# Kernel tuning notes

Measured on AMD Instinct MI355X. Metric: run time of the kernel, lower is better.

Reference implementation:

```python
import jax, jax.numpy as jnp
import numpy as np

GAMMA = 0.5
SCALE_BASE = 512.0
LN_EPS = 1e-5


def _xpos(x, downscale=False):
    # x: (B, S, Dh); RetNet XPOS rotary embedding (Jamie-Stirling impl)
    S, Dh = x.shape[1], x.shape[2]
    half = Dh // 2
    base_scale = (jnp.arange(0, Dh, 2, dtype=jnp.float32) + 0.4 * Dh) / (1.4 * Dh)  # (half,)
    power = jnp.arange(S, dtype=jnp.float32)[:, None] / SCALE_BASE                   # (S,1)
    scale = base_scale[None, :] ** power                                             # (S,half)
    inv_freq = 1.0 / (10000.0 ** (jnp.arange(half, dtype=jnp.float32) / half))       # (half,)
    sinusoid = jnp.arange(S, dtype=jnp.float32)[:, None] * inv_freq[None, :]         # (S,half)
    sin, cos = jnp.sin(sinusoid), jnp.cos(sinusoid)
    if downscale:
        scale = 1.0 / scale
    # duplicate_interleave: (S,half) -> (S,Dh) repeating each column twice
    sin_s = jnp.repeat(sin * scale, 2, axis=-1)
    cos_s = jnp.repeat(cos * scale, 2, axis=-1)
    x1, x2 = x[..., ::2], x[..., 1::2]
    rot = jnp.stack((-x2, x1), axis=-1).reshape(x.shape)  # rotate_every_two
    return x * cos_s + rot * sin_s


def _decay_mask(S):
    n = jnp.arange(S)
    diff = (n[:, None] - n[None, :]).astype(jnp.float32)
    return jnp.where(n[:, None] >= n[None, :], GAMMA ** diff, 0.0)  # (S,S)


def setup_inputs() -> dict:
    key = jax.random.key(0)
    ks = jax.random.split(key, 10)
    D, d = 768, 192
    hw, b, s = 196, 8, 32
    x = jax.random.normal(ks[0], (hw, b * s, D), dtype=jnp.float32)
    scale_in = 1.0 / np.sqrt(D)
    scale_d = 1.0 / np.sqrt(d)
    return {
        "x": x,
        "W1": jax.random.normal(ks[1], (D, d), dtype=jnp.float32) * scale_in,
        "b1": jnp.zeros((d,), dtype=jnp.float32),
        "W2": jax.random.normal(ks[2], (d, D), dtype=jnp.float32) * scale_d,
        "b2": jnp.zeros((D,), dtype=jnp.float32),
        "ln_g": jnp.ones((d,), dtype=jnp.float32),
        "ln_b": jnp.zeros((d,), dtype=jnp.float32),
        "WQ": jax.random.normal(ks[3], (d, d), dtype=jnp.float32) * scale_d,
        "WK": jax.random.normal(ks[4], (d, d), dtype=jnp.float32) * scale_d,
        "WV": jax.random.normal(ks[5], (d, d), dtype=jnp.float32) * scale_d,
        "batch_dim": 8,
        "seq_dim": 32,
        "hw": 196,
    }


def reference(x, W1, b1, W2, b2, ln_g, ln_b, WQ, WK, WV, batch_dim, seq_dim, hw):
    D = x.shape[-1]
    # (hw, b*s, D) -> (b*hw, s, D)
    xr = x.reshape(hw, batch_dim, seq_dim, D).transpose(1, 0, 2, 3)
    xr = xr.reshape(batch_dim * hw, seq_dim, D)
    x_down = xr @ W1 + b1  # (B, s, d)
    # LayerNorm
    mu = jnp.mean(x_down, axis=-1, keepdims=True)
    var = jnp.mean((x_down - mu) ** 2, axis=-1, keepdims=True)
    h = (x_down - mu) / jnp.sqrt(var + LN_EPS) * ln_g + ln_b
    # SimpleRetention (parallel form)
    Q = _xpos(h @ WQ, downscale=False)
    K = _xpos(h @ WK, downscale=True)
    V = h @ WV
    Dmask = _decay_mask(seq_dim)  # (s,s)
    att = jnp.einsum("bnd,bmd->bnm", Q, K) * Dmask[None]
    ret = att @ V  # (B, s, d)
    out = xr + (ret @ W2 + b2)
    # (b*hw, s, D) -> (hw, b*s, D)
    out = out.reshape(batch_dim, hw, seq_dim, D).transpose(1, 0, 2, 3)
    return out.reshape(hw, batch_dim * seq_dim, D)
```

## Files before the change

kernel.cpp:

```cpp
#include <hip/hip_runtime.h>

typedef __bf16 bf16x8 __attribute__((ext_vector_type(8)));
typedef __bf16 bf16x4 __attribute__((ext_vector_type(4)));
typedef float floatx4 __attribute__((ext_vector_type(4)));

__device__ __forceinline__ __bf16 f2bf(float f) {
  union { float f; unsigned u; } x; x.f = f;
  unsigned r = (x.u + 0x7FFFu + ((x.u >> 16) & 1u)) >> 16;
  union { unsigned short u; __bf16 b; } o; o.u = (unsigned short)r; return o.b;
}
__device__ __forceinline__ float bf2f(__bf16 b) {
  union { unsigned short u; __bf16 b; } i; i.b = b;
  union { unsigned u; float f; } y; y.u = ((unsigned)i.u) << 16; return y.f;
}

#define MFMA16(a, b, c) __builtin_amdgcn_mfma_f32_16x16x32_bf16(a, b, c, 0, 0, 0)

__global__ __launch_bounds__(256) void prep_weights(
    const float* __restrict__ W1, const float* __restrict__ WQ,
    const float* __restrict__ WK, const float* __restrict__ WV,
    const float* __restrict__ W2,
    __bf16* __restrict__ w1f, __bf16* __restrict__ wqf,
    __bf16* __restrict__ wkf, __bf16* __restrict__ wvf,
    __bf16* __restrict__ w2f) {
  int i = blockIdx.x * 256 + threadIdx.x;
  if (i < 147456) {
    int e = i & 7, lane = (i >> 3) & 63, rest = i >> 9;
    int kk32 = rest % 24, nt = rest / 24;
    int n = nt * 16 + (lane & 15), k = kk32 * 32 + (lane >> 4) * 8 + e;
    w1f[i] = f2bf(W1[k * 192 + n]); return;
  }
  i -= 147456;
  if (i < 36864) {
    int e = i & 7, lane = (i >> 3) & 63, rest = i >> 9;
    int kk32 = rest % 6, nt = rest / 6;
    int n = nt * 16 + (lane & 15), k = kk32 * 32 + (lane >> 4) * 8 + e;
    wqf[i] = f2bf(WQ[k * 192 + n]); return;
  }
  i -= 36864;
  if (i < 36864) {
    int e = i & 7, lane = (i >> 3) & 63, rest = i >> 9;
    int kk32 = rest % 6, nt = rest / 6;
    int n = nt * 16 + (lane & 15), k = kk32 * 32 + (lane >> 4) * 8 + e;
    wkf[i] = f2bf(WK[k * 192 + n]); return;
  }
  i -= 36864;
  if (i < 36864) {
    int e = i & 7, lane = (i >> 3) & 63, rest = i >> 9;
    int kk32 = rest % 6, nt = rest / 6;
    int n = nt * 16 + (lane & 15), k = kk32 * 32 + (lane >> 4) * 8 + e;
    wvf[i] = f2bf(WV[k * 192 + n]); return;
  }
  i -= 36864;
  if (i < 147456) {
    int e = i & 7, lane = (i >> 3) & 63, rest = i >> 9;
    int kk32 = rest % 6, nt = rest / 6;
    int n = nt * 16 + (lane & 15), k = kk32 * 32 + (lane >> 4) * 8 + e;
    w2f[i] = f2bf(W2[k * 768 + n]); return;
  }
}

__global__ __launch_bounds__(256) void prep_xf(
    const float* __restrict__ x, __bf16* __restrict__ xf) {
  int j = blockIdx.x * 256 + threadIdx.x;
  int lane = j & 63;
  int rest = j >> 6;
  int kk32 = rest % 24;
  int rest2 = rest / 24;
  size_t row = (size_t)rest2 * 16 + (lane & 15);
  int d = kk32 * 32 + ((lane >> 4) & 3) * 8;
  const float* src = x + row * 768 + d;
  float4 f0 = *(const float4*)(src);
  float4 f1 = *(const float4*)(src + 4);
  bf16x8 a;
  a[0] = f2bf(f0.x); a[1] = f2bf(f0.y); a[2] = f2bf(f0.z); a[3] = f2bf(f0.w);
  a[4] = f2bf(f1.x); a[5] = f2bf(f1.y); a[6] = f2bf(f1.z); a[7] = f2bf(f1.w);
  *(bf16x8*)(xf + (size_t)j * 8) = a;
}

__global__ __launch_bounds__(256) void prep_tables(
    float* __restrict__ cq, float* __restrict__ sq,
    float* __restrict__ ck, float* __restrict__ sk) {
  int i = blockIdx.x * 256 + threadIdx.x;
  if (i >= 32 * 96) return;
  int s = i / 96, f = i % 96;
  float base = (2.f * f + 0.4f * 192.f) / (1.4f * 192.f);
  float scale = powf(base, (float)s / 512.f);
  float invf = powf(10000.f, -(float)f / 96.f);
  float ang = (float)s * invf;
  float sn = sinf(ang), cs = cosf(ang);
  int o = s * 192 + 2 * f;
  cq[o] = cs * scale; cq[o + 1] = cs * scale;
  sq[o] = sn * scale; sq[o + 1] = sn * scale;
  ck[o] = cs / scale; ck[o + 1] = cs / scale;
  sk[o] = sn / scale; sk[o + 1] = sn / scale;
}

#define SW(r, c) ((r) * 192 + ((c) ^ (((r) & 7) << 3)))

template <bool USE_XF>
__global__ __launch_bounds__(256) void retnet_main(
    const float* __restrict__ x, const float* __restrict__ b1,
    const float* __restrict__ b2, const float* __restrict__ ln_g,
    const float* __restrict__ ln_b,
    const __bf16* __restrict__ w1f, const __bf16* __restrict__ wqf,
    const __bf16* __restrict__ wkf, const __bf16* __restrict__ wvf,
    const __bf16* __restrict__ w2f,
    const float* __restrict__ cq, const float* __restrict__ sq,
    const float* __restrict__ ck, const float* __restrict__ sk,
    const __bf16* __restrict__ xf, float* __restrict__ out) {
  __shared__ __align__(16) char smem[51200];
  __bf16* Q = (__bf16*)smem;
  __bf16* Kl = (__bf16*)(smem + 12288);
  __bf16* Vt = (__bf16*)(smem + 24576);
  __bf16* att = (__bf16*)(smem + 36864);
  __bf16* h = (__bf16*)(smem + 38912);

  const int tid = threadIdx.x;
  const int wv = tid >> 6;
  const int lane = tid & 63;
  const int l16 = lane & 15;
  const int quad = lane >> 4;
  const int kof = quad * 8;
  const int p = blockIdx.x;
  const float* xblk = x + (size_t)p * 32 * 768;

  {
    floatx4 acc[2][3] = {};
    if (USE_XF) {
      const __bf16* xfp = xf + (size_t)p * 24576;
#pragma unroll 4
      for (int kk32 = 0; kk32 < 24; ++kk32) {
        bf16x8 a0 = *(const bf16x8*)(xfp + kk32 * 512 + lane * 8);
        bf16x8 a1 = *(const bf16x8*)(xfp + 12288 + kk32 * 512 + lane * 8);
#pragma unroll
        for (int t = 0; t < 3; ++t) {
          bf16x8 bb = *(const bf16x8*)(w1f + (size_t)((wv * 3 + t) * 24 + kk32) * 512 + lane * 8);
          acc[0][t] = MFMA16(a0, bb, acc[0][t]);
          acc[1][t] = MFMA16(a1, bb, acc[1][t]);
        }
      }
    } else {
      const float* arow0 = xblk + l16 * 768;
      const float* arow1 = xblk + (16 + l16) * 768;
#pragma unroll 2
      for (int kk = 0; kk < 768; kk += 32) {
        float4 f0 = *(const float4*)(arow0 + kk + kof);
        float4 f1 = *(const float4*)(arow0 + kk + kof + 4);
        float4 g0 = *(const float4*)(arow1 + kk + kof);
        float4 g1 = *(const float4*)(arow1 + kk + kof + 4);
        bf16x8 a0, a1;
        a0[0] = f2bf(f0.x); a0[1] = f2bf(f0.y); a0[2] = f2bf(f0.z); a0[3] = f2bf(f0.w);
        a0[4] = f2bf(f1.x); a0[5] = f2bf(f1.y); a0[6] = f2bf(f1.z); a0[7] = f2bf(f1.w);
        a1[0] = f2bf(g0.x); a1[1] = f2bf(g0.y); a1[2] = f2bf(g0.z); a1[3] = f2bf(g0.w);
        a1[4] = f2bf(g1.x); a1[5] = f2bf(g1.y); a1[6] = f2bf(g1.z); a1[7] = f2bf(g1.w);
        int kk32 = kk >> 5;
#pragma unroll
        for (int t = 0; t < 3; ++t) {
          bf16x8 bb = *(const bf16x8*)(w1f + (size_t)((wv * 3 + t) * 24 + kk32) * 512 + lane * 8);
          acc[0][t] = MFMA16(a0, bb, acc[0][t]);
          acc[1][t] = MFMA16(a1, bb, acc[1][t]);
        }
      }
    }
#pragma unroll
    for (int m = 0; m < 2; ++m)
#pragma unroll
      for (int t = 0; t < 3; ++t) {
        int col = wv * 48 + t * 16 + l16;
        float bias = b1[col];
#pragma unroll
        for (int r = 0; r < 4; ++r) {
          int row = m * 16 + quad * 4 + r;
          h[SW(row, col)] = f2bf(acc[m][t][r] + bias);
        }
      }
  }
  __syncthreads();

  {
    int r = tid >> 3, g = tid & 7;
    float vals[24]; float s = 0.f, s2 = 0.f;
#pragma unroll
    for (int j = 0; j < 24; ++j) {
      int c = g * 24 + j;
      float v = bf2f(h[SW(r, c)]);
      vals[j] = v; s += v; s2 += v * v;
    }
#pragma unroll
    for (int o = 1; o < 8; o <<= 1) { s += __shfl_xor(s, o); s2 += __shfl_xor(s2, o); }
    float mu = s * (1.f / 192.f);
    float var = s2 * (1.f / 192.f) - mu * mu;
    float rstd = rsqrtf(var + 1e-5f);
#pragma unroll
    for (int j = 0; j < 24; ++j) {
      int c = g * 24 + j;
      h[SW(r, c)] = f2bf((vals[j] - mu) * rstd * ln_g[c] + ln_b[c]);
    }
  }
  __syncthreads();

  auto gemm_h = [&](const __bf16* __restrict__ Wf, floatx4 (&acc)[2][3]) {
#pragma unroll
    for (int kk32 = 0; kk32 < 6; ++kk32) {
      bf16x8 a0 = *(const bf16x8*)(h + SW(l16, kk32 * 32 + kof));
      bf16x8 a1 = *(const bf16x8*)(h + SW(16 + l16, kk32 * 32 + kof));
#pragma unroll
      for (int t = 0; t < 3; ++t) {
        bf16x8 bb = *(const bf16x8*)(Wf + (size_t)((wv * 3 + t) * 6 + kk32) * 512 + lane * 8);
        acc[0][t] = MFMA16(a0, bb, acc[0][t]);
        acc[1][t] = MFMA16(a1, bb, acc[1][t]);
      }
    }
  };
  {
    floatx4 acc[2][3] = {};
    gemm_h(wqf, acc);
#pragma unroll
    for (int m = 0; m < 2; ++m)
#pragma unroll
      for (int t = 0; t < 3; ++t) {
        int col = wv * 48 + t * 16 + l16;
#pragma unroll
        for (int r = 0; r < 4; ++r) {
          int row = m * 16 + quad * 4 + r;
          float v = acc[m][t][r];
          float pr = __shfl_xor(v, 1);
          float o = v * cq[row * 192 + col] + ((lane & 1) ? pr : -pr) * sq[row * 192 + col];
          Q[SW(row, col)] = f2bf(o);
        }
      }
  }
  {
    floatx4 acc[2][3] = {};
    gemm_h(wkf, acc);
#pragma unroll
    for (int m = 0; m < 2; ++m)
#pragma unroll
      for (int t = 0; t < 3; ++t) {
        int col = wv * 48 + t * 16 + l16;
#pragma unroll
        for (int r = 0; r < 4; ++r) {
          int row = m * 16 + quad * 4 + r;
          float v = acc[m][t][r];
          float pr = __shfl_xor(v, 1);
          float o = v * ck[row * 192 + col] + ((lane & 1) ? pr : -pr) * sk[row * 192 + col];
          Kl[SW(row, col)] = f2bf(o);
        }
      }
  }
  {
    floatx4 acc[2][3] = {};
    gemm_h(wvf, acc);
#pragma unroll
    for (int m = 0; m < 2; ++m)
#pragma unroll
      for (int t = 0; t < 3; ++t) {
        int col = wv * 48 + t * 16 + l16;
        bf16x4 pk;
#pragma unroll
        for (int r = 0; r < 4; ++r) pk[r] = f2bf(acc[m][t][r]);
        *(bf16x4*)(Vt + col * 32 + m * 16 + quad * 4) = pk;
      }
  }
  __syncthreads();

  {
    int mt = wv >> 1, nt = wv & 1;
    floatx4 acc = {0.f, 0.f, 0.f, 0.f};
#pragma unroll
    for (int kk = 0; kk < 192; kk += 32) {
      bf16x8 a = *(const bf16x8*)(Q + SW(mt * 16 + l16, kk + kof));
      bf16x8 bb = *(const bf16x8*)(Kl + SW(nt * 16 + l16, kk + kof));
      acc = MFMA16(a, bb, acc);
    }
#pragma unroll
    for (int r = 0; r < 4; ++r) {
      int i = mt * 16 + quad * 4 + r;
      int j = nt * 16 + l16;
      float v = (i >= j) ? acc[r] * exp2f((float)(j - i)) : 0.f;
      att[i * 32 + j] = f2bf(v);
    }
  }
  __syncthreads();

  {
    floatx4 acc[2][3] = {};
    bf16x8 a0 = *(const bf16x8*)(att + l16 * 32 + kof);
    bf16x8 a1 = *(const bf16x8*)(att + (16 + l16) * 32 + kof);
#pragma unroll
    for (int t = 0; t < 3; ++t) {
      bf16x8 bb = *(const bf16x8*)(Vt + (wv * 48 + t * 16 + l16) * 32 + kof);
      acc[0][t] = MFMA16(a0, bb, acc[0][t]);
      acc[1][t] = MFMA16(a1, bb, acc[1][t]);
    }
#pragma unroll
    for (int m = 0; m < 2; ++m)
#pragma unroll
      for (int t = 0; t < 3; ++t) {
        int col = wv * 48 + t * 16 + l16;
#pragma unroll
        for (int r = 0; r < 4; ++r) {
          int row = m * 16 + quad * 4 + r;
          h[SW(row, col)] = f2bf(acc[m][t][r]);
        }
      }
  }
  __syncthreads();

  {
    bf16x8 af[2][6];
#pragma unroll
    for (int k6 = 0; k6 < 6; ++k6) {
      af[0][k6] = *(const bf16x8*)(h + SW(l16, k6 * 32 + kof));
      af[1][k6] = *(const bf16x8*)(h + SW(16 + l16, k6 * 32 + kof));
    }
#pragma unroll
    for (int g = 0; g < 4; ++g) {
      floatx4 acc[2][3] = {};
#pragma unroll
      for (int k6 = 0; k6 < 6; ++k6) {
#pragma unroll
        for (int t = 0; t < 3; ++t) {
          bf16x8 bb = *(const bf16x8*)(w2f + (size_t)((wv * 12 + g * 3 + t) * 6 + k6) * 512 + lane * 8);
          acc[0][t] = MFMA16(af[0][k6], bb, acc[0][t]);
          acc[1][t] = MFMA16(af[1][k6], bb, acc[1][t]);
        }
      }
#pragma unroll
      for (int m = 0; m < 2; ++m)
#pragma unroll
        for (int t = 0; t < 3; ++t) {
          int col = wv * 192 + g * 48 + t * 16 + l16;
          float bias = b2[col];
#pragma unroll
          for (int r = 0; r < 4; ++r) {
            int row = m * 16 + quad * 4 + r;
            size_t gi = (size_t)p * 24576 + row * 768 + col;
            out[gi] = xblk[row * 768 + col] + acc[m][t][r] + bias;
          }
        }
    }
  }
}

extern "C" void kernel_launch(void* const* d_in, const int* in_sizes, int n_in,
                              void* d_out, int out_size, void* d_ws, size_t ws_size,
                              hipStream_t stream) {
  const float* x = (const float*)d_in[0];
  const float* W1 = (const float*)d_in[1];
  const float* b1 = (const float*)d_in[2];
  const float* W2 = (const float*)d_in[3];
  const float* b2 = (const float*)d_in[4];
  const float* lng = (const float*)d_in[5];
  const float* lnb = (const float*)d_in[6];
  const float* WQ = (const float*)d_in[7];
  const float* WK = (const float*)d_in[8];
  const float* WV = (const float*)d_in[9];
  float* out = (float*)d_out;

  char* ws = (char*)d_ws;
  __bf16* w1f = (__bf16*)(ws + 0);
  __bf16* wqf = (__bf16*)(ws + 294912);
  __bf16* wkf = (__bf16*)(ws + 368640);
  __bf16* wvf = (__bf16*)(ws + 442368);
  __bf16* w2f = (__bf16*)(ws + 516096);
  float* cq = (float*)(ws + 811008);
  float* sq = cq + 6144;
  float* ck = sq + 6144;
  float* sk = ck + 6144;
  const size_t xf_off = 909312;
  const size_t xf_bytes = 77070336;
  bool use_xf = (ws_size >= xf_off + xf_bytes);
  __bf16* xfp = (__bf16*)(ws + xf_off);

  hipLaunchKernelGGL(prep_weights, dim3(1584), dim3(256), 0, stream,
                     W1, WQ, WK, WV, W2, w1f, wqf, wkf, wvf, w2f);
  hipLaunchKernelGGL(prep_tables, dim3(12), dim3(256), 0, stream, cq, sq, ck, sk);
  if (use_xf) {
    hipLaunchKernelGGL(prep_xf, dim3(18816), dim3(256), 0, stream, x, xfp);
    hipLaunchKernelGGL((retnet_main<true>), dim3(1568), dim3(256), 0, stream,
                       x, b1, b2, lng, lnb, w1f, wqf, wkf, wvf, w2f,
                       cq, sq, ck, sk, (const __bf16*)xfp, out);
  } else {
    hipLaunchKernelGGL((retnet_main<false>), dim3(1568), dim3(256), 0, stream,
                       x, b1, b2, lng, lnb, w1f, wqf, wkf, wvf, w2f,
                       cq, sq, ck, sk, (const __bf16*)nullptr, out);
  }
}
```

Before: 452.0 us.

## Fuse x bf16 conversion into main kernel with double-buffered LDS staging

Drops the separate prep_xf pass, which wrote a bf16 copy of x to workspace and read it back. The main kernel now loads fp32 x in chunks, converts it, and stages it into LDS in MFMA fragment order, double-buffered across the Q/K regions so the next chunk's global loads overlap the current chunk's MFMAs. All LDS tiles switch from swizzled row-major to a fragment-native layout, the attention matrix reuses the Q buffer so LDS shrinks, and launch bounds request 3 blocks per CU. The cost is extra barriers inside the first GEMM and more register pressure from the in-flight loads.

```diff
diff --git a/kernel.cpp b/kernel.cpp
--- a/kernel.cpp
+++ b/kernel.cpp
@@ -12,6 +12,17 @@
 __device__ __forceinline__ float bf2f(__bf16 b) {
   union { unsigned short u; __bf16 b; } i; i.b = b;
   union { unsigned u; float f; } y; y.u = ((unsigned)i.u) << 16; return y.f;
+}
+__device__ __forceinline__ bf16x8 cvt8(float4 f0, float4 f1) {
+  bf16x8 v;
+  v[0] = f2bf(f0.x); v[1] = f2bf(f0.y); v[2] = f2bf(f0.z); v[3] = f2bf(f0.w);
+  v[4] = f2bf(f1.x); v[5] = f2bf(f1.y); v[6] = f2bf(f1.z); v[7] = f2bf(f1.w);
+  return v;
+}
+
+__device__ __forceinline__ int afoff(int row, int col, int Kb) {
+  return ((((row >> 4) * Kb + (col >> 5)) * 64 + ((col >> 3) & 3) * 16 + (row & 15)) << 4)
+         + ((col & 7) << 1);
 }
 
 #define MFMA16(a, b, c) __builtin_amdgcn_mfma_f32_16x16x32_bf16(a, b, c, 0, 0, 0)
@@ -58,24 +69,6 @@
     int n = nt * 16 + (lane & 15), k = kk32 * 32 + (lane >> 4) * 8 + e;
     w2f[i] = f2bf(W2[k * 768 + n]); return;
   }
-}
-
-__global__ __launch_bounds__(256) void prep_xf(
-    const float* __restrict__ x, __bf16* __restrict__ xf) {
-  int j = blockIdx.x * 256 + threadIdx.x;
-  int lane = j & 63;
-  int rest = j >> 6;
-  int kk32 = rest % 24;
-  int rest2 = rest / 24;
-  size_t row = (size_t)rest2 * 16 + (lane & 15);
-  int d = kk32 * 32 + ((lane >> 4) & 3) * 8;
-  const float* src = x + row * 768 + d;
-  float4 f0 = *(const float4*)(src);
-  float4 f1 = *(const float4*)(src + 4);
-  bf16x8 a;
-  a[0] = f2bf(f0.x); a[1] = f2bf(f0.y); a[2] = f2bf(f0.z); a[3] = f2bf(f0.w);
-  a[4] = f2bf(f1.x); a[5] = f2bf(f1.y); a[6] = f2bf(f1.z); a[7] = f2bf(f1.w);
-  *(bf16x8*)(xf + (size_t)j * 8) = a;
 }
 
 __global__ __launch_bounds__(256) void prep_tables(
@@ -96,10 +89,7 @@
   sk[o] = sn / scale; sk[o + 1] = sn / scale;
 }
 
-#define SW(r, c) ((r) * 192 + ((c) ^ (((r) & 7) << 3)))
-
-template <bool USE_XF>
-__global__ __launch_bounds__(256) void retnet_main(
+__global__ __launch_bounds__(256, 3) void retnet_main(
     const float* __restrict__ x, const float* __restrict__ b1,
     const float* __restrict__ b2, const float* __restrict__ ln_g,
     const float* __restrict__ ln_b,
@@ -108,59 +98,72 @@
     const __bf16* __restrict__ w2f,
     const float* __restrict__ cq, const float* __restrict__ sq,
     const float* __restrict__ ck, const float* __restrict__ sk,
-    const __bf16* __restrict__ xf, float* __restrict__ out) {
-  __shared__ __align__(16) char smem[51200];
-  __bf16* Q = (__bf16*)smem;
-  __bf16* Kl = (__bf16*)(smem + 12288);
-  __bf16* Vt = (__bf16*)(smem + 24576);
-  __bf16* att = (__bf16*)(smem + 36864);
-  __bf16* h = (__bf16*)(smem + 38912);
+    float* __restrict__ out) {
+  __shared__ __align__(16) char smem[49152];
+  char* Qb = smem;
+  char* Kb = smem + 12288;
+  char* Vtb = smem + 24576;
+  char* hb = smem + 36864;
 
   const int tid = threadIdx.x;
   const int wv = tid >> 6;
   const int lane = tid & 63;
   const int l16 = lane & 15;
   const int quad = lane >> 4;
-  const int kof = quad * 8;
+  const int lane16 = lane << 4;
+  const int wv3 = wv * 3;
   const int p = blockIdx.x;
-  const float* xblk = x + (size_t)p * 32 * 768;
-
-  {
-    floatx4 acc[2][3] = {};
-    if (USE_XF) {
-      const __bf16* xfp = xf + (size_t)p * 24576;
-#pragma unroll 4
-      for (int kk32 = 0; kk32 < 24; ++kk32) {
-        bf16x8 a0 = *(const bf16x8*)(xfp + kk32 * 512 + lane * 8);
-        bf16x8 a1 = *(const bf16x8*)(xfp + 12288 + kk32 * 512 + lane * 8);
+  const float* xblk = x + (size_t)p * 24576;
+
+  const int srow = tid >> 3;
+  const int scol8 = (tid & 7) * 8;
+  const float* sbase = xblk + srow * 768 + scol8;
+  const int wo0 = ((((srow >> 4) * 6 + (scol8 >> 5)) * 64 +
+                    ((scol8 >> 3) & 3) * 16 + (srow & 15)) << 4);
+  const char* w1b = (const char*)w1f;
+
+  floatx4 acc[2][3] = {};
+  {
+    {
+      float4 L[6];
+#pragma unroll
+      for (int g = 0; g < 3; ++g) {
+        const float* a = sbase + g * 64;
+        L[2 * g] = *(const float4*)a; L[2 * g + 1] = *(const float4*)(a + 4);
+      }
+#pragma unroll
+      for (int g = 0; g < 3; ++g)
+        *(bf16x8*)(Qb + wo0 + g * 2048) = cvt8(L[2 * g], L[2 * g + 1]);
+    }
+    __syncthreads();
+#pragma unroll
+    for (int c = 0; c < 4; ++c) {
+      char* rb = (c & 1) ? Kb : Qb;
+      char* wb = (c & 1) ? Qb : Kb;
+      float4 L[6];
+      if (c < 3) {
+#pragma unroll
+        for (int g = 0; g < 3; ++g) {
+          const float* a = sbase + (c + 1) * 192 + g * 64;
+          L[2 * g] = *(const float4*)a; L[2 * g + 1] = *(const float4*)(a + 4);
+        }
+      }
+#pragma unroll
+      for (int kkc = 0; kkc < 6; ++kkc) {
+        bf16x8 a0 = *(const bf16x8*)(rb + kkc * 1024 + lane16);
+        bf16x8 a1 = *(const bf16x8*)(rb + (6 + kkc) * 1024 + lane16);
 #pragma unroll
         for (int t = 0; t < 3; ++t) {
-          bf16x8 bb = *(const bf16x8*)(w1f + (size_t)((wv * 3 + t) * 24 + kk32) * 512 + lane * 8);
+          bf16x8 bb = *(const bf16x8*)(w1b + (size_t)((wv3 + t) * 24 + c * 6 + kkc) * 1024 + lane16);
           acc[0][t] = MFMA16(a0, bb, acc[0][t]);
           acc[1][t] = MFMA16(a1, bb, acc[1][t]);
         }
       }
-    } else {
-      const float* arow0 = xblk + l16 * 768;
-      const float* arow1 = xblk + (16 + l16) * 768;
-#pragma unroll 2
-      for (int kk = 0; kk < 768; kk += 32) {
-        float4 f0 = *(const float4*)(arow0 + kk + kof);
-        float4 f1 = *(const float4*)(arow0 + kk + kof + 4);
-        float4 g0 = *(const float4*)(arow1 + kk + kof);
-        float4 g1 = *(const float4*)(arow1 + kk + kof + 4);
-        bf16x8 a0, a1;
-        a0[0] = f2bf(f0.x); a0[1] = f2bf(f0.y); a0[2] = f2bf(f0.z); a0[3] = f2bf(f0.w);
-        a0[4] = f2bf(f1.x); a0[5] = f2bf(f1.y); a0[6] = f2bf(f1.z); a0[7] = f2bf(f1.w);
-        a1[0] = f2bf(g0.x); a1[1] = f2bf(g0.y); a1[2] = f2bf(g0.z); a1[3] = f2bf(g0.w);
-        a1[4] = f2bf(g1.x); a1[5] = f2bf(g1.y); a1[6] = f2bf(g1.z); a1[7] = f2bf(g1.w);
-        int kk32 = kk >> 5;
-#pragma unroll
-        for (int t = 0; t < 3; ++t) {
-          bf16x8 bb = *(const bf16x8*)(w1f + (size_t)((wv * 3 + t) * 24 + kk32) * 512 + lane * 8);
-          acc[0][t] = MFMA16(a0, bb, acc[0][t]);
-          acc[1][t] = MFMA16(a1, bb, acc[1][t]);
-        }
+      if (c < 3) {
+#pragma unroll
+        for (int g = 0; g < 3; ++g)
+          *(bf16x8*)(wb + wo0 + g * 2048) = cvt8(L[2 * g], L[2 * g + 1]);
+        __syncthreads();
       }
     }
 #pragma unroll
@@ -172,7 +175,7 @@
 #pragma unroll
         for (int r = 0; r < 4; ++r) {
           int row = m * 16 + quad * 4 + r;
-          h[SW(row, col)] = f2bf(acc[m][t][r] + bias);
+          *(__bf16*)(hb + afoff(row, col, 6)) = f2bf(acc[m][t][r] + bias);
         }
       }
   }
@@ -184,7 +187,7 @@
 #pragma unroll
     for (int j = 0; j < 24; ++j) {
       int c = g * 24 + j;
-      float v = bf2f(h[SW(r, c)]);
+      float v = bf2f(*(const __bf16*)(hb + afoff(r, c, 6)));
       vals[j] = v; s += v; s2 += v * v;
     }
 #pragma unroll
@@ -195,27 +198,28 @@
 #pragma unroll
     for (int j = 0; j < 24; ++j) {
       int c = g * 24 + j;
-      h[SW(r, c)] = f2bf((vals[j] - mu) * rstd * ln_g[c] + ln_b[c]);
-    }
-  }
-  __syncthreads();
-
-  auto gemm_h = [&](const __bf16* __restrict__ Wf, floatx4 (&acc)[2][3]) {
-#pragma unroll
-    for (int kk32 = 0; kk32 < 6; ++kk32) {
-      bf16x8 a0 = *(const bf16x8*)(h + SW(l16, kk32 * 32 + kof));
-      bf16x8 a1 = *(const bf16x8*)(h + SW(16 + l16, kk32 * 32 + kof));
-#pragma unroll
-      for (int t = 0; t < 3; ++t) {
-        bf16x8 bb = *(const bf16x8*)(Wf + (size_t)((wv * 3 + t) * 6 + kk32) * 512 + lane * 8);
-        acc[0][t] = MFMA16(a0, bb, acc[0][t]);
-        acc[1][t] = MFMA16(a1, bb, acc[1][t]);
+      *(__bf16*)(hb + afoff(r, c, 6)) = f2bf((vals[j] - mu) * rstd * ln_g[c] + ln_b[c]);
+    }
+  }
+  __syncthreads();
+
+  auto gemm_h = [&](const __bf16* __restrict__ Wf, floatx4(&a)[2][3]) {
+    const char* wc = (const char*)Wf;
+#pragma unroll
+    for (int kk = 0; kk < 6; ++kk) {
+      bf16x8 a0 = *(const bf16x8*)(hb + kk * 1024 + lane16);
+      bf16x8 a1 = *(const bf16x8*)(hb + (6 + kk) * 1024 + lane16);
+#pragma unroll
+      for (int t = 0; t < 3; ++t) {
+        bf16x8 bb = *(const bf16x8*)(wc + (size_t)((wv3 + t) * 6 + kk) * 1024 + lane16);
+        a[0][t] = MFMA16(a0, bb, a[0][t]);
+        a[1][t] = MFMA16(a1, bb, a[1][t]);
       }
     }
   };
   {
-    floatx4 acc[2][3] = {};
-    gemm_h(wqf, acc);
+    floatx4 aq[2][3] = {};
+    gemm_h(wqf, aq);
 #pragma unroll
     for (int m = 0; m < 2; ++m)
 #pragma unroll
@@ -224,16 +228,16 @@
 #pragma unroll
         for (int r = 0; r < 4; ++r) {
           int row = m * 16 + quad * 4 + r;
-          float v = acc[m][t][r];
+          float v = aq[m][t][r];
           float pr = __shfl_xor(v, 1);
           float o = v * cq[row * 192 + col] + ((lane & 1) ? pr : -pr) * sq[row * 192 + col];
-          Q[SW(row, col)] = f2bf(o);
-        }
-      }
-  }
-  {
-    floatx4 acc[2][3] = {};
-    gemm_h(wkf, acc);
+          *(__bf16*)(Qb + afoff(row, col, 6)) = f2bf(o);
+        }
+      }
+  }
+  {
+    floatx4 ak[2][3] = {};
+    gemm_h(wkf, ak);
 #pragma unroll
     for (int m = 0; m < 2; ++m)
 #pragma unroll
@@ -242,57 +246,59 @@
 #pragma unroll
         for (int r = 0; r < 4; ++r) {
           int row = m * 16 + quad * 4 + r;
-          float v = acc[m][t][r];
+          float v = ak[m][t][r];
           float pr = __shfl_xor(v, 1);
           float o = v * ck[row * 192 + col] + ((lane & 1) ? pr : -pr) * sk[row * 192 + col];
-          Kl[SW(row, col)] = f2bf(o);
-        }
-      }
-  }
-  {
-    floatx4 acc[2][3] = {};
-    gemm_h(wvf, acc);
-#pragma unroll
-    for (int m = 0; m < 2; ++m)
-#pragma unroll
-      for (int t = 0; t < 3; ++t) {
-        int col = wv * 48 + t * 16 + l16;
+          *(__bf16*)(Kb + afoff(row, col, 6)) = f2bf(o);
+        }
+      }
+  }
+  {
+    floatx4 av[2][3] = {};
+    gemm_h(wvf, av);
+#pragma unroll
+    for (int m = 0; m < 2; ++m)
+#pragma unroll
+      for (int t = 0; t < 3; ++t) {
+        int d = wv * 48 + t * 16 + l16;
+        int s0 = m * 16 + quad * 4;
         bf16x4 pk;
 #pragma unroll
-        for (int r = 0; r < 4; ++r) pk[r] = f2bf(acc[m][t][r]);
-        *(bf16x4*)(Vt + col * 32 + m * 16 + quad * 4) = pk;
+        for (int r = 0; r < 4; ++r) pk[r] = f2bf(av[m][t][r]);
+        *(bf16x4*)(Vtb + afoff(d, s0, 1)) = pk;
       }
   }
   __syncthreads();
 
   {
     int mt = wv >> 1, nt = wv & 1;
-    floatx4 acc = {0.f, 0.f, 0.f, 0.f};
-#pragma unroll
-    for (int kk = 0; kk < 192; kk += 32) {
-      bf16x8 a = *(const bf16x8*)(Q + SW(mt * 16 + l16, kk + kof));
-      bf16x8 bb = *(const bf16x8*)(Kl + SW(nt * 16 + l16, kk + kof));
-      acc = MFMA16(a, bb, acc);
-    }
+    floatx4 a4 = {0.f, 0.f, 0.f, 0.f};
+#pragma unroll
+    for (int kk = 0; kk < 6; ++kk) {
+      bf16x8 a = *(const bf16x8*)(Qb + (mt * 6 + kk) * 1024 + lane16);
+      bf16x8 bb = *(const bf16x8*)(Kb + (nt * 6 + kk) * 1024 + lane16);
+      a4 = MFMA16(a, bb, a4);
+    }
+    __syncthreads();
 #pragma unroll
     for (int r = 0; r < 4; ++r) {
       int i = mt * 16 + quad * 4 + r;
       int j = nt * 16 + l16;
-      float v = (i >= j) ? acc[r] * exp2f((float)(j - i)) : 0.f;
-      att[i * 32 + j] = f2bf(v);
-    }
-  }
-  __syncthreads();
-
-  {
-    floatx4 acc[2][3] = {};
-    bf16x8 a0 = *(const bf16x8*)(att + l16 * 32 + kof);
-    bf16x8 a1 = *(const bf16x8*)(att + (16 + l16) * 32 + kof);
+      float v = (i >= j) ? a4[r] * exp2f((float)(j - i)) : 0.f;
+      *(__bf16*)(Qb + afoff(i, j, 1)) = f2bf(v);
+    }
+  }
+  __syncthreads();
+
+  {
+    floatx4 ar[2][3] = {};
+    bf16x8 a0 = *(const bf16x8*)(Qb + lane16);
+    bf16x8 a1 = *(const bf16x8*)(Qb + 1024 + lane16);
 #pragma unroll
     for (int t = 0; t < 3; ++t) {
-      bf16x8 bb = *(const bf16x8*)(Vt + (wv * 48 + t * 16 + l16) * 32 + kof);
-      acc[0][t] = MFMA16(a0, bb, acc[0][t]);
-      acc[1][t] = MFMA16(a1, bb, acc[1][t]);
+      bf16x8 bb = *(const bf16x8*)(Vtb + (wv3 + t) * 1024 + lane16);
+      ar[0][t] = MFMA16(a0, bb, ar[0][t]);
+      ar[1][t] = MFMA16(a1, bb, ar[1][t]);
     }
 #pragma unroll
     for (int m = 0; m < 2; ++m)
@@ -302,29 +308,30 @@
 #pragma unroll
         for (int r = 0; r < 4; ++r) {
           int row = m * 16 + quad * 4 + r;
-          h[SW(row, col)] = f2bf(acc[m][t][r]);
-        }
-      }
-  }
-  __syncthreads();
-
-  {
+          *(__bf16*)(hb + afoff(row, col, 6)) = f2bf(ar[m][t][r]);
+        }
+      }
+  }
+  __syncthreads();
+
+  {
+    const char* w2b = (const char*)w2f;
     bf16x8 af[2][6];
 #pragma unroll
     for (int k6 = 0; k6 < 6; ++k6) {
-      af[0][k6] = *(const bf16x8*)(h + SW(l16, k6 * 32 + kof));
-      af[1][k6] = *(const bf16x8*)(h + SW(16 + l16, k6 * 32 + kof));
+      af[0][k6] = *(const bf16x8*)(hb + k6 * 1024 + lane16);
+      af[1][k6] = *(const bf16x8*)(hb + (6 + k6) * 1024 + lane16);
     }
 #pragma unroll
     for (int g = 0; g < 4; ++g) {
-      floatx4 acc[2][3] = {};
+      floatx4 ao[2][3] = {};
 #pragma unroll
       for (int k6 = 0; k6 < 6; ++k6) {
 #pragma unroll
         for (int t = 0; t < 3; ++t) {
-          bf16x8 bb = *(const bf16x8*)(w2f + (size_t)((wv * 12 + g * 3 + t) * 6 + k6) * 512 + lane * 8);
-          acc[0][t] = MFMA16(af[0][k6], bb, acc[0][t]);
-          acc[1][t] = MFMA16(af[1][k6], bb, acc[1][t]);
+          bf16x8 bb = *(const bf16x8*)(w2b + (size_t)((wv * 12 + g * 3 + t) * 6 + k6) * 1024 + lane16);
+          ao[0][t] = MFMA16(af[0][k6], bb, ao[0][t]);
+          ao[1][t] = MFMA16(af[1][k6], bb, ao[1][t]);
         }
       }
 #pragma unroll
@@ -337,7 +344,7 @@
           for (int r = 0; r < 4; ++r) {
             int row = m * 16 + quad * 4 + r;
             size_t gi = (size_t)p * 24576 + row * 768 + col;
-            out[gi] = xblk[row * 768 + col] + acc[m][t][r] + bias;
+            out[gi] = xblk[row * 768 + col] + ao[m][t][r] + bias;
           }
         }
     }
@@ -369,22 +376,11 @@
   float* sq = cq + 6144;
   float* ck = sq + 6144;
   float* sk = ck + 6144;
-  const size_t xf_off = 909312;
-  const size_t xf_bytes = 77070336;
-  bool use_xf = (ws_size >= xf_off + xf_bytes);
-  __bf16* xfp = (__bf16*)(ws + xf_off);
 
   hipLaunchKernelGGL(prep_weights, dim3(1584), dim3(256), 0, stream,
                      W1, WQ, WK, WV, W2, w1f, wqf, wkf, wvf, w2f);
   hipLaunchKernelGGL(prep_tables, dim3(12), dim3(256), 0, stream, cq, sq, ck, sk);
-  if (use_xf) {
-    hipLaunchKernelGGL(prep_xf, dim3(18816), dim3(256), 0, stream, x, xfp);
-    hipLaunchKernelGGL((retnet_main<true>), dim3(1568), dim3(256), 0, stream,
-                       x, b1, b2, lng, lnb, w1f, wqf, wkf, wvf, w2f,
-                       cq, sq, ck, sk, (const __bf16*)xfp, out);
-  } else {
-    hipLaunchKernelGGL((retnet_main<false>), dim3(1568), dim3(256), 0, stream,
-                       x, b1, b2, lng, lnb, w1f, wqf, wkf, wvf, w2f,
-                       cq, sq, ck, sk, (const __bf16*)nullptr, out);
-  }
-}
+  hipLaunchKernelGGL(retnet_main, dim3(1568), dim3(256), 0, stream,
+                     x, b1, b2, lng, lnb, w1f, wqf, wkf, wvf, w2f,
+                     cq, sq, ck, sk, out);
+}
```

New measurement: 525.3 us. 1.16x slower.

## Process two sequences per block and stage prep_xf through shared memory

Applied to the files above, without the earlier changes.

The main kernel now handles two 32-row sequences per workgroup, so each weight fragment loaded from global memory feeds twice as many MFMAs. LDS buffers are doubled and reused across phases (V and h share storage, ret and Q share storage), and V is held in registers across a barrier. prep_xf now reads each 32x768 tile with coalesced float4 loads into a swizzled LDS tile, then writes it out in fragment order. Trade-offs: larger LDS use (about 78 KB) and more registers can lower occupancy, and the grid halves to 784 blocks.

```diff
diff --git a/kernel.cpp b/kernel.cpp
--- a/kernel.cpp
+++ b/kernel.cpp
@@ -15,6 +15,9 @@
 }
 
 #define MFMA16(a, b, c) __builtin_amdgcn_mfma_f32_16x16x32_bf16(a, b, c, 0, 0, 0)
+
+#define SW(r, c) ((r) * 192 + ((c) ^ (((r) & 7) << 3)))
+#define SWX(r, c) ((r) * 768 + ((c) ^ (((r) & 7) << 3)))
 
 __global__ __launch_bounds__(256) void prep_weights(
     const float* __restrict__ W1, const float* __restrict__ WQ,
@@ -62,20 +65,30 @@
 
 __global__ __launch_bounds__(256) void prep_xf(
     const float* __restrict__ x, __bf16* __restrict__ xf) {
-  int j = blockIdx.x * 256 + threadIdx.x;
-  int lane = j & 63;
-  int rest = j >> 6;
-  int kk32 = rest % 24;
-  int rest2 = rest / 24;
-  size_t row = (size_t)rest2 * 16 + (lane & 15);
-  int d = kk32 * 32 + ((lane >> 4) & 3) * 8;
-  const float* src = x + row * 768 + d;
-  float4 f0 = *(const float4*)(src);
-  float4 f1 = *(const float4*)(src + 4);
-  bf16x8 a;
-  a[0] = f2bf(f0.x); a[1] = f2bf(f0.y); a[2] = f2bf(f0.z); a[3] = f2bf(f0.w);
-  a[4] = f2bf(f1.x); a[5] = f2bf(f1.y); a[6] = f2bf(f1.z); a[7] = f2bf(f1.w);
-  *(bf16x8*)(xf + (size_t)j * 8) = a;
+  __shared__ __align__(16) __bf16 tile[24576];
+  int p = blockIdx.x;
+  int tid = threadIdx.x;
+  const float* xb = x + (size_t)p * 24576;
+#pragma unroll
+  for (int i = 0; i < 24; ++i) {
+    int idx = i * 256 + tid;
+    float4 v = ((const float4*)xb)[idx];
+    int row = idx / 192, c4 = (idx % 192) * 4;
+    bf16x4 b;
+    b[0] = f2bf(v.x); b[1] = f2bf(v.y); b[2] = f2bf(v.z); b[3] = f2bf(v.w);
+    *(bf16x4*)(&tile[SWX(row, c4)]) = b;
+  }
+  __syncthreads();
+  __bf16* dst = xf + (size_t)p * 24576;
+#pragma unroll
+  for (int w = 0; w < 12; ++w) {
+    int j = w * 256 + tid;
+    int lane = j & 63, rest = j >> 6;
+    int kk32 = rest % 24, mt = rest / 24;
+    int row = mt * 16 + (lane & 15);
+    int col = kk32 * 32 + ((lane >> 4) & 3) * 8;
+    *(bf16x8*)(dst + j * 8) = *(const bf16x8*)(&tile[SWX(row, col)]);
+  }
 }
 
 __global__ __launch_bounds__(256) void prep_tables(
@@ -96,10 +109,8 @@
   sk[o] = sn / scale; sk[o + 1] = sn / scale;
 }
 
-#define SW(r, c) ((r) * 192 + ((c) ^ (((r) & 7) << 3)))
-
 template <bool USE_XF>
-__global__ __launch_bounds__(256) void retnet_main(
+__global__ __launch_bounds__(256, 2) void retnet_main(
     const float* __restrict__ x, const float* __restrict__ b1,
     const float* __restrict__ b2, const float* __restrict__ ln_g,
     const float* __restrict__ ln_b,
@@ -109,12 +120,13 @@
     const float* __restrict__ cq, const float* __restrict__ sq,
     const float* __restrict__ ck, const float* __restrict__ sk,
     const __bf16* __restrict__ xf, float* __restrict__ out) {
-  __shared__ __align__(16) char smem[51200];
-  __bf16* Q = (__bf16*)smem;
-  __bf16* Kl = (__bf16*)(smem + 12288);
-  __bf16* Vt = (__bf16*)(smem + 24576);
-  __bf16* att = (__bf16*)(smem + 36864);
-  __bf16* h = (__bf16*)(smem + 38912);
+  __shared__ __align__(16) char smem[79872];
+  __bf16* h[2] = {(__bf16*)smem, (__bf16*)(smem + 12288)};
+  __bf16* Q[2] = {(__bf16*)(smem + 24576), (__bf16*)(smem + 36864)};
+  __bf16* K[2] = {(__bf16*)(smem + 49152), (__bf16*)(smem + 61440)};
+  __bf16* att[2] = {(__bf16*)(smem + 73728), (__bf16*)(smem + 76800)};
+  __bf16** Vt = h;
+  __bf16** ret = Q;
 
   const int tid = threadIdx.x;
   const int wv = tid >> 6;
@@ -122,224 +134,267 @@
   const int l16 = lane & 15;
   const int quad = lane >> 4;
   const int kof = quad * 8;
+  const int wv3 = wv * 3;
   const int p = blockIdx.x;
-  const float* xblk = x + (size_t)p * 32 * 768;
-
-  {
-    floatx4 acc[2][3] = {};
+  const float* xblk[2] = {x + (size_t)(2 * p) * 24576, x + (size_t)(2 * p + 1) * 24576};
+
+  {
+    floatx4 acc[2][2][3] = {};
     if (USE_XF) {
-      const __bf16* xfp = xf + (size_t)p * 24576;
+      const __bf16* xf0 = xf + (size_t)(2 * p) * 24576;
 #pragma unroll 4
       for (int kk32 = 0; kk32 < 24; ++kk32) {
-        bf16x8 a0 = *(const bf16x8*)(xfp + kk32 * 512 + lane * 8);
-        bf16x8 a1 = *(const bf16x8*)(xfp + 12288 + kk32 * 512 + lane * 8);
-#pragma unroll
-        for (int t = 0; t < 3; ++t) {
-          bf16x8 bb = *(const bf16x8*)(w1f + (size_t)((wv * 3 + t) * 24 + kk32) * 512 + lane * 8);
-          acc[0][t] = MFMA16(a0, bb, acc[0][t]);
-          acc[1][t] = MFMA16(a1, bb, acc[1][t]);
+        bf16x8 a[2][2];
+#pragma unroll
+        for (int ss = 0; ss < 2; ++ss) {
+          a[ss][0] = *(const bf16x8*)(xf0 + ss * 24576 + kk32 * 512 + lane * 8);
+          a[ss][1] = *(const bf16x8*)(xf0 + ss * 24576 + 12288 + kk32 * 512 + lane * 8);
+        }
+#pragma unroll
+        for (int t = 0; t < 3; ++t) {
+          bf16x8 bb = *(const bf16x8*)(w1f + (size_t)((wv3 + t) * 24 + kk32) * 512 + lane * 8);
+          acc[0][0][t] = MFMA16(a[0][0], bb, acc[0][0][t]);
+          acc[0][1][t] = MFMA16(a[0][1], bb, acc[0][1][t]);
+          acc[1][0][t] = MFMA16(a[1][0], bb, acc[1][0][t]);
+          acc[1][1][t] = MFMA16(a[1][1], bb, acc[1][1][t]);
         }
       }
     } else {
-      const float* arow0 = xblk + l16 * 768;
-      const float* arow1 = xblk + (16 + l16) * 768;
 #pragma unroll 2
       for (int kk = 0; kk < 768; kk += 32) {
-        float4 f0 = *(const float4*)(arow0 + kk + kof);
-        float4 f1 = *(const float4*)(arow0 + kk + kof + 4);
-        float4 g0 = *(const float4*)(arow1 + kk + kof);
-        float4 g1 = *(const float4*)(arow1 + kk + kof + 4);
-        bf16x8 a0, a1;
-        a0[0] = f2bf(f0.x); a0[1] = f2bf(f0.y); a0[2] = f2bf(f0.z); a0[3] = f2bf(f0.w);
-        a0[4] = f2bf(f1.x); a0[5] = f2bf(f1.y); a0[6] = f2bf(f1.z); a0[7] = f2bf(f1.w);
-        a1[0] = f2bf(g0.x); a1[1] = f2bf(g0.y); a1[2] = f2bf(g0.z); a1[3] = f2bf(g0.w);
-        a1[4] = f2bf(g1.x); a1[5] = f2bf(g1.y); a1[6] = f2bf(g1.z); a1[7] = f2bf(g1.w);
+        bf16x8 a[2][2];
+#pragma unroll
+        for (int ss = 0; ss < 2; ++ss)
+#pragma unroll
+          for (int m = 0; m < 2; ++m) {
+            const float* ar = xblk[ss] + (m * 16 + l16) * 768 + kk + kof;
+            float4 f0 = *(const float4*)ar;
+            float4 f1 = *(const float4*)(ar + 4);
+            bf16x8 v;
+            v[0] = f2bf(f0.x); v[1] = f2bf(f0.y); v[2] = f2bf(f0.z); v[3] = f2bf(f0.w);
+            v[4] = f2bf(f1.x); v[5] = f2bf(f1.y); v[6] = f2bf(f1.z); v[7] = f2bf(f1.w);
+            a[ss][m] = v;
+          }
         int kk32 = kk >> 5;
 #pragma unroll
         for (int t = 0; t < 3; ++t) {
-          bf16x8 bb = *(const bf16x8*)(w1f + (size_t)((wv * 3 + t) * 24 + kk32) * 512 + lane * 8);
-          acc[0][t] = MFMA16(a0, bb, acc[0][t]);
-          acc[1][t] = MFMA16(a1, bb, acc[1][t]);
-        }
-      }
-    }
-#pragma unroll
-    for (int m = 0; m < 2; ++m)
-#pragma unroll
-      for (int t = 0; t < 3; ++t) {
-        int col = wv * 48 + t * 16 + l16;
-        float bias = b1[col];
-#pragma unroll
-        for (int r = 0; r < 4; ++r) {
-          int row = m * 16 + quad * 4 + r;
-          h[SW(row, col)] = f2bf(acc[m][t][r] + bias);
-        }
-      }
-  }
-  __syncthreads();
-
-  {
-    int r = tid >> 3, g = tid & 7;
-    float vals[24]; float s = 0.f, s2 = 0.f;
-#pragma unroll
-    for (int j = 0; j < 24; ++j) {
-      int c = g * 24 + j;
-      float v = bf2f(h[SW(r, c)]);
-      vals[j] = v; s += v; s2 += v * v;
-    }
-#pragma unroll
-    for (int o = 1; o < 8; o <<= 1) { s += __shfl_xor(s, o); s2 += __shfl_xor(s2, o); }
-    float mu = s * (1.f / 192.f);
-    float var = s2 * (1.f / 192.f) - mu * mu;
-    float rstd = rsqrtf(var + 1e-5f);
-#pragma unroll
-    for (int j = 0; j < 24; ++j) {
-      int c = g * 24 + j;
-      h[SW(r, c)] = f2bf((vals[j] - mu) * rstd * ln_g[c] + ln_b[c]);
-    }
-  }
-  __syncthreads();
-
-  auto gemm_h = [&](const __bf16* __restrict__ Wf, floatx4 (&acc)[2][3]) {
-#pragma unroll
-    for (int kk32 = 0; kk32 < 6; ++kk32) {
-      bf16x8 a0 = *(const bf16x8*)(h + SW(l16, kk32 * 32 + kof));
-      bf16x8 a1 = *(const bf16x8*)(h + SW(16 + l16, kk32 * 32 + kof));
-#pragma unroll
-      for (int t = 0; t < 3; ++t) {
-        bf16x8 bb = *(const bf16x8*)(Wf + (size_t)((wv * 3 + t) * 6 + kk32) * 512 + lane * 8);
-        acc[0][t] = MFMA16(a0, bb, acc[0][t]);
-        acc[1][t] = MFMA16(a1, bb, acc[1][t]);
-      }
-    }
-  };
-  {
-    floatx4 acc[2][3] = {};
-    gemm_h(wqf, acc);
-#pragma unroll
-    for (int m = 0; m < 2; ++m)
-#pragma unroll
-      for (int t = 0; t < 3; ++t) {
-        int col = wv * 48 + t * 16 + l16;
-#pragma unroll
-        for (int r = 0; r < 4; ++r) {
-          int row = m * 16 + quad * 4 + r;
-          float v = acc[m][t][r];
-          float pr = __shfl_xor(v, 1);
-          float o = v * cq[row * 192 + col] + ((lane & 1) ? pr : -pr) * sq[row * 192 + col];
-          Q[SW(row, col)] = f2bf(o);
-        }
-      }
-  }
-  {
-    floatx4 acc[2][3] = {};
-    gemm_h(wkf, acc);
-#pragma unroll
-    for (int m = 0; m < 2; ++m)
-#pragma unroll
-      for (int t = 0; t < 3; ++t) {
-        int col = wv * 48 + t * 16 + l16;
-#pragma unroll
-        for (int r = 0; r < 4; ++r) {
-          int row = m * 16 + quad * 4 + r;
-          float v = acc[m][t][r];
-          float pr = __shfl_xor(v, 1);
-          float o = v * ck[row * 192 + col] + ((lane & 1) ? pr : -pr) * sk[row * 192 + col];
-          Kl[SW(row, col)] = f2bf(o);
-        }
-      }
-  }
-  {
-    floatx4 acc[2][3] = {};
-    gemm_h(wvf, acc);
-#pragma unroll
-    for (int m = 0; m < 2; ++m)
-#pragma unroll
-      for (int t = 0; t < 3; ++t) {
-        int col = wv * 48 + t * 16 + l16;
-        bf16x4 pk;
-#pragma unroll
-        for (int r = 0; r < 4; ++r) pk[r] = f2bf(acc[m][t][r]);
-        *(bf16x4*)(Vt + col * 32 + m * 16 + quad * 4) = pk;
-      }
-  }
-  __syncthreads();
-
-  {
-    int mt = wv >> 1, nt = wv & 1;
-    floatx4 acc = {0.f, 0.f, 0.f, 0.f};
-#pragma unroll
-    for (int kk = 0; kk < 192; kk += 32) {
-      bf16x8 a = *(const bf16x8*)(Q + SW(mt * 16 + l16, kk + kof));
-      bf16x8 bb = *(const bf16x8*)(Kl + SW(nt * 16 + l16, kk + kof));
-      acc = MFMA16(a, bb, acc);
-    }
-#pragma unroll
-    for (int r = 0; r < 4; ++r) {
-      int i = mt * 16 + quad * 4 + r;
-      int j = nt * 16 + l16;
-      float v = (i >= j) ? acc[r] * exp2f((float)(j - i)) : 0.f;
-      att[i * 32 + j] = f2bf(v);
-    }
-  }
-  __syncthreads();
-
-  {
-    floatx4 acc[2][3] = {};
-    bf16x8 a0 = *(const bf16x8*)(att + l16 * 32 + kof);
-    bf16x8 a1 = *(const bf16x8*)(att + (16 + l16) * 32 + kof);
-#pragma unroll
-    for (int t = 0; t < 3; ++t) {
-      bf16x8 bb = *(const bf16x8*)(Vt + (wv * 48 + t * 16 + l16) * 32 + kof);
-      acc[0][t] = MFMA16(a0, bb, acc[0][t]);
-      acc[1][t] = MFMA16(a1, bb, acc[1][t]);
-    }
-#pragma unroll
-    for (int m = 0; m < 2; ++m)
-#pragma unroll
-      for (int t = 0; t < 3; ++t) {
-        int col = wv * 48 + t * 16 + l16;
-#pragma unroll
-        for (int r = 0; r < 4; ++r) {
-          int row = m * 16 + quad * 4 + r;
-          h[SW(row, col)] = f2bf(acc[m][t][r]);
-        }
-      }
-  }
-  __syncthreads();
-
-  {
-    bf16x8 af[2][6];
-#pragma unroll
-    for (int k6 = 0; k6 < 6; ++k6) {
-      af[0][k6] = *(const bf16x8*)(h + SW(l16, k6 * 32 + kof));
-      af[1][k6] = *(const bf16x8*)(h + SW(16 + l16, k6 * 32 + kof));
-    }
-#pragma unroll
-    for (int g = 0; g < 4; ++g) {
-      floatx4 acc[2][3] = {};
-#pragma unroll
-      for (int k6 = 0; k6 < 6; ++k6) {
-#pragma unroll
-        for (int t = 0; t < 3; ++t) {
-          bf16x8 bb = *(const bf16x8*)(w2f + (size_t)((wv * 12 + g * 3 + t) * 6 + k6) * 512 + lane * 8);
-          acc[0][t] = MFMA16(af[0][k6], bb, acc[0][t]);
-          acc[1][t] = MFMA16(af[1][k6], bb, acc[1][t]);
-        }
-      }
-#pragma unroll
-      for (int m = 0; m < 2; ++m)
-#pragma unroll
-        for (int t = 0; t < 3; ++t) {
-          int col = wv * 192 + g * 48 + t * 16 + l16;
-          float bias = b2[col];
+          bf16x8 bb = *(const bf16x8*)(w1f + (size_t)((wv3 + t) * 24 + kk32) * 512 + lane * 8);
+          acc[0][0][t] = MFMA16(a[0][0], bb, acc[0][0][t]);
+          acc[0][1][t] = MFMA16(a[0][1], bb, acc[0][1][t]);
+          acc[1][0][t] = MFMA16(a[1][0], bb, acc[1][0][t]);
+          acc[1][1][t] = MFMA16(a[1][1], bb, acc[1][1][t]);
+        }
+      }
+    }
+#pragma unroll
+    for (int ss = 0; ss < 2; ++ss)
+#pragma unroll
+      for (int m = 0; m < 2; ++m)
+#pragma unroll
+        for (int t = 0; t < 3; ++t) {
+          int col = wv * 48 + t * 16 + l16;
+          float bias = b1[col];
 #pragma unroll
           for (int r = 0; r < 4; ++r) {
             int row = m * 16 + quad * 4 + r;
-            size_t gi = (size_t)p * 24576 + row * 768 + col;
-            out[gi] = xblk[row * 768 + col] + acc[m][t][r] + bias;
-          }
-        }
+            h[ss][SW(row, col)] = f2bf(acc[ss][m][t][r] + bias);
+          }
+        }
+  }
+  __syncthreads();
+
+  {
+    int r = tid >> 3, g = tid & 7;
+#pragma unroll
+    for (int ss = 0; ss < 2; ++ss) {
+      float vals[24]; float s = 0.f, s2 = 0.f;
+#pragma unroll
+      for (int j = 0; j < 24; ++j) {
+        int c = g * 24 + j;
+        float v = bf2f(h[ss][SW(r, c)]);
+        vals[j] = v; s += v; s2 += v * v;
+      }
+#pragma unroll
+      for (int o = 1; o < 8; o <<= 1) { s += __shfl_xor(s, o); s2 += __shfl_xor(s2, o); }
+      float mu = s * (1.f / 192.f);
+      float var = s2 * (1.f / 192.f) - mu * mu;
+      float rstd = rsqrtf(var + 1e-5f);
+#pragma unroll
+      for (int j = 0; j < 24; ++j) {
+        int c = g * 24 + j;
+        h[ss][SW(r, c)] = f2bf((vals[j] - mu) * rstd * ln_g[c] + ln_b[c]);
+      }
+    }
+  }
+  __syncthreads();
+
+  auto gemm_h2 = [&](const __bf16* __restrict__ Wf, floatx4 (&a)[2][2][3]) {
+#pragma unroll
+    for (int kk = 0; kk < 6; ++kk) {
+      bf16x8 a00 = *(const bf16x8*)(h[0] + SW(l16, kk * 32 + kof));
+      bf16x8 a01 = *(const bf16x8*)(h[0] + SW(16 + l16, kk * 32 + kof));
+      bf16x8 a10 = *(const bf16x8*)(h[1] + SW(l16, kk * 32 + kof));
+      bf16x8 a11 = *(const bf16x8*)(h[1] + SW(16 + l16, kk * 32 + kof));
+#pragma unroll
+      for (int t = 0; t < 3; ++t) {
+        bf16x8 bb = *(const bf16x8*)(Wf + (size_t)((wv3 + t) * 6 + kk) * 512 + lane * 8);
+        a[0][0][t] = MFMA16(a00, bb, a[0][0][t]);
+        a[0][1][t] = MFMA16(a01, bb, a[0][1][t]);
+        a[1][0][t] = MFMA16(a10, bb, a[1][0][t]);
+        a[1][1][t] = MFMA16(a11, bb, a[1][1][t]);
+      }
+    }
+  };
+  bf16x4 vv[2][2][3];
+  {
+    floatx4 aq[2][2][3] = {};
+    gemm_h2(wqf, aq);
+#pragma unroll
+    for (int ss = 0; ss < 2; ++ss)
+#pragma unroll
+      for (int m = 0; m < 2; ++m)
+#pragma unroll
+        for (int t = 0; t < 3; ++t) {
+          int col = wv * 48 + t * 16 + l16;
+#pragma unroll
+          for (int r = 0; r < 4; ++r) {
+            int row = m * 16 + quad * 4 + r;
+            float v = aq[ss][m][t][r];
+            float pr = __shfl_xor(v, 1);
+            float o = v * cq[row * 192 + col] + ((lane & 1) ? pr : -pr) * sq[row * 192 + col];
+            Q[ss][SW(row, col)] = f2bf(o);
+          }
+        }
+  }
+  {
+    floatx4 ak[2][2][3] = {};
+    gemm_h2(wkf, ak);
+#pragma unroll
+    for (int ss = 0; ss < 2; ++ss)
+#pragma unroll
+      for (int m = 0; m < 2; ++m)
+#pragma unroll
+        for (int t = 0; t < 3; ++t) {
+          int col = wv * 48 + t * 16 + l16;
+#pragma unroll
+          for (int r = 0; r < 4; ++r) {
+            int row = m * 16 + quad * 4 + r;
+            float v = ak[ss][m][t][r];
+            float pr = __shfl_xor(v, 1);
+            float o = v * ck[row * 192 + col] + ((lane & 1) ? pr : -pr) * sk[row * 192 + col];
+            K[ss][SW(row, col)] = f2bf(o);
+          }
+        }
+  }
+  {
+    floatx4 av[2][2][3] = {};
+    gemm_h2(wvf, av);
+#pragma unroll
+    for (int ss = 0; ss < 2; ++ss)
+#pragma unroll
+      for (int m = 0; m < 2; ++m)
+#pragma unroll
+        for (int t = 0; t < 3; ++t)
+#pragma unroll
+          for (int r = 0; r < 4; ++r) vv[ss][m][t][r] = f2bf(av[ss][m][t][r]);
+  }
+  __syncthreads();
+
+  {
+#pragma unroll
+    for (int ss = 0; ss < 2; ++ss)
+#pragma unroll
+      for (int m = 0; m < 2; ++m)
+#pragma unroll
+        for (int t = 0; t < 3; ++t) {
+          int col = wv * 48 + t * 16 + l16;
+          *(bf16x4*)(Vt[ss] + col * 32 + m * 16 + quad * 4) = vv[ss][m][t];
+        }
+    int mt = wv >> 1, nt = wv & 1;
+#pragma unroll
+    for (int ss = 0; ss < 2; ++ss) {
+      floatx4 a4 = {0.f, 0.f, 0.f, 0.f};
+#pragma unroll
+      for (int kk = 0; kk < 6; ++kk) {
+        bf16x8 aq = *(const bf16x8*)(Q[ss] + SW(mt * 16 + l16, kk * 32 + kof));
+        bf16x8 bk = *(const bf16x8*)(K[ss] + SW(nt * 16 + l16, kk * 32 + kof));
+        a4 = MFMA16(aq, bk, a4);
+      }
+#pragma unroll
+      for (int r = 0; r < 4; ++r) {
+        int i = mt * 16 + quad * 4 + r;
+        int j = nt * 16 + l16;
+        float v = (i >= j) ? a4[r] * exp2f((float)(j - i)) : 0.f;
+        att[ss][i * 48 + j] = f2bf(v);
+      }
+    }
+  }
+  __syncthreads();
+
+  {
+#pragma unroll
+    for (int ss = 0; ss < 2; ++ss) {
+      floatx4 ar[2][3] = {};
+      bf16x8 a0 = *(const bf16x8*)(att[ss] + l16 * 48 + kof);
+      bf16x8 a1 = *(const bf16x8*)(att[ss] + (16 + l16) * 48 + kof);
+#pragma unroll
+      for (int t = 0; t < 3; ++t) {
+        bf16x8 bb = *(const bf16x8*)(Vt[ss] + (wv * 48 + t * 16 + l16) * 32 + kof);
+        ar[0][t] = MFMA16(a0, bb, ar[0][t]);
+        ar[1][t] = MFMA16(a1, bb, ar[1][t]);
+      }
+#pragma unroll
+      for (int m = 0; m < 2; ++m)
+#pragma unroll
+        for (int t = 0; t < 3; ++t) {
+          int col = wv * 48 + t * 16 + l16;
+#pragma unroll
+          for (int r = 0; r < 4; ++r) {
+            int row = m * 16 + quad * 4 + r;
+            ret[ss][SW(row, col)] = f2bf(ar[m][t][r]);
+          }
+        }
+    }
+  }
+  __syncthreads();
+
+  {
+    bf16x8 af[2][2][6];
+#pragma unroll
+    for (int ss = 0; ss < 2; ++ss)
+#pragma unroll
+      for (int k6 = 0; k6 < 6; ++k6) {
+        af[ss][0][k6] = *(const bf16x8*)(ret[ss] + SW(l16, k6 * 32 + kof));
+        af[ss][1][k6] = *(const bf16x8*)(ret[ss] + SW(16 + l16, k6 * 32 + kof));
+      }
+#pragma unroll
+    for (int g = 0; g < 4; ++g) {
+      floatx4 ao[2][2][3] = {};
+#pragma unroll
+      for (int k6 = 0; k6 < 6; ++k6)
+#pragma unroll
+        for (int t = 0; t < 3; ++t) {
+          bf16x8 bb = *(const bf16x8*)(w2f + (size_t)((wv * 12 + g * 3 + t) * 6 + k6) * 512 + lane * 8);
+          ao[0][0][t] = MFMA16(af[0][0][k6], bb, ao[0][0][t]);
+          ao[0][1][t] = MFMA16(af[0][1][k6], bb, ao[0][1][t]);
+          ao[1][0][t] = MFMA16(af[1][0][k6], bb, ao[1][0][t]);
+          ao[1][1][t] = MFMA16(af[1][1][k6], bb, ao[1][1][t]);
+        }
+#pragma unroll
+      for (int ss = 0; ss < 2; ++ss)
+#pragma unroll
+        for (int m = 0; m < 2; ++m)
+#pragma unroll
+          for (int t = 0; t < 3; ++t) {
+            int col = wv * 192 + g * 48 + t * 16 + l16;
+            float bias = b2[col];
+#pragma unroll
+            for (int r = 0; r < 4; ++r) {
+              int row = m * 16 + quad * 4 + r;
+              size_t gi = (size_t)(2 * p + ss) * 24576 + row * 768 + col;
+              out[gi] = xblk[ss][row * 768 + col] + ao[ss][m][t][r] + bias;
+            }
+          }
     }
   }
 }
@@ -378,12 +433,12 @@
                      W1, WQ, WK, WV, W2, w1f, wqf, wkf, wvf, w2f);
   hipLaunchKernelGGL(prep_tables, dim3(12), dim3(256), 0, stream, cq, sq, ck, sk);
   if (use_xf) {
-    hipLaunchKernelGGL(prep_xf, dim3(18816), dim3(256), 0, stream, x, xfp);
-    hipLaunchKernelGGL((retnet_main<true>), dim3(1568), dim3(256), 0, stream,
+    hipLaunchKernelGGL(prep_xf, dim3(1568), dim3(256), 0, stream, x, xfp);
+    hipLaunchKernelGGL((retnet_main<true>), dim3(784), dim3(256), 0, stream,
                        x, b1, b2, lng, lnb, w1f, wqf, wkf, wvf, w2f,
                        cq, sq, ck, sk, (const __bf16*)xfp, out);
   } else {
-    hipLaunchKernelGGL((retnet_main<false>), dim3(1568), dim3(256), 0, stream,
+    hipLaunchKernelGGL((retnet_main<false>), dim3(784), dim3(256), 0, stream,
                        x, b1, b2, lng, lnb, w1f, wqf, wkf, wvf, w2f,
                        cq, sq, ck, sk, (const __bf16*)nullptr, out);
   }
```

Measured after the change: 598.6 us. 32.4% more time.
